# Kernel optimization log

Hardware: AMD Instinct MI355X
Metric: run time of the kernel (lower is better)

## Reference

```python
import jax, jax.numpy as jnp
import numpy as np

B, T, D = 2, 1024, 2048
E, K, H = 64, 4, 512          # n_experts, top-k, expert_dim
S, HS = 2, H * K              # shared experts, shared hidden dim
CAP = 512


def setup_inputs() -> dict:
    key = jax.random.key(0)
    ks = jax.random.split(key, 9)
    scale = 0.02
    return {
        "x": jax.random.normal(ks[0], (B, T, D), jnp.float32),
        "Wr": jax.random.normal(ks[1], (D, E), jnp.float32) * scale,
        "router_bias": jnp.zeros((E,), jnp.float32),
        "Wg": jax.random.normal(ks[2], (E, D, H), jnp.float32) * scale,
        "Wu": jax.random.normal(ks[3], (E, D, H), jnp.float32) * scale,
        "Wd": jax.random.normal(ks[4], (E, H, D), jnp.float32) * scale,
        "Sg": jax.random.normal(ks[5], (S, D, HS), jnp.float32) * scale,
        "Su": jax.random.normal(ks[6], (S, D, HS), jnp.float32) * scale,
        "Sd": jax.random.normal(ks[7], (S, HS, D), jnp.float32) * scale,
    }


def reference(x, Wr, router_bias, Wg, Wu, Wd, Sg, Su, Sd):
    Bx, Tx, Dx = x.shape
    N = Bx * Tx
    flat = x.reshape(N, Dx)                              # [N, D]

    # ---- router ----
    logits = flat @ Wr + router_bias                     # [N, E]
    scores = jax.nn.softmax(logits, axis=-1)
    topk_scores, topk_idx = jax.lax.top_k(scores, K)     # [N, K]
    topk_scores = topk_scores / topk_scores.sum(-1, keepdims=True)

    eid = topk_idx.reshape(-1)                           # [N*K] expert per assignment
    w = topk_scores.reshape(-1)                          # [N*K] combine weight
    tok = jnp.repeat(jnp.arange(N), K)                   # [N*K] source token id

    # position of each assignment within its expert's buffer
    oh = jax.nn.one_hot(eid, E, dtype=jnp.int32)         # [N*K, E]
    pos = ((jnp.cumsum(oh, axis=0) * oh).sum(-1) - 1)    # [N*K]
    valid = pos < CAP

    # ---- dispatch: scatter tokens into per-expert buffers ----
    xb = jnp.zeros((E, CAP, Dx), x.dtype).at[eid, pos].set(flat[tok], mode="drop")

    # ---- grouped SwiGLU expert FFN ----
    h = jax.nn.silu(jnp.einsum("ecd,edh->ech", xb, Wg)) * jnp.einsum("ecd,edh->ech", xb, Wu)
    yb = jnp.einsum("ech,ehd->ecd", h, Wd)               # [E, CAP, D]

    # ---- combine: gather back and weighted scatter-add to tokens ----
    y = yb[eid, jnp.minimum(pos, CAP - 1)] * (w * valid)[:, None]
    out = jnp.zeros((N, Dx), x.dtype).at[tok].add(y)

    # ---- always-on shared experts ----
    hs = jax.nn.silu(jnp.einsum("nd,sdh->nsh", flat, Sg)) * jnp.einsum("nd,sdh->nsh", flat, Su)
    out = out + jnp.einsum("nsh,shd->nd", hs, Sd)

    return out.reshape(Bx, Tx, Dx)
```

## Files before the change

### kernel.cpp

```cpp
#include <hip/hip_runtime.h>
#include <hip/hip_bf16.h>
#include <stdint.h>

#define N_TOK 2048
#define DM    2048
#define NEXP  64
#define TOPK  4
#define HEXP  512
#define CAPC  512
#define NSH   2
#define HSH   2048
#define RTB   8

typedef __attribute__((ext_vector_type(8))) short short8;
typedef __attribute__((ext_vector_type(4))) float f32x4;
typedef __attribute__((ext_vector_type(4))) float f4;
typedef __attribute__((ext_vector_type(4))) unsigned uint4v;

#define GLDS16(g, l) __builtin_amdgcn_global_load_lds(                     \
    (const __attribute__((address_space(1))) void*)(g),                    \
    (__attribute__((address_space(3))) void*)(l), 16, 0, 0)

#define VMWAIT(N) asm volatile("s_waitcnt vmcnt(" #N ")" ::: "memory")
#define BARX() do { asm volatile("" ::: "memory");                          \
                    __builtin_amdgcn_s_barrier();                           \
                    asm volatile("" ::: "memory"); } while (0)

static __device__ __forceinline__ unsigned short f2bf(float f) {
  union { float f; unsigned u; } v; v.f = f;
  unsigned r = v.u + 0x7FFFu + ((v.u >> 16) & 1u);
  return (unsigned short)(r >> 16);
}

static __device__ __forceinline__ int swz_xcd(int id, int nwg) {
  return (id & 7) * (nwg >> 3) + (id >> 3);
}

__global__ __launch_bounds__(256) void k_convert(const float* __restrict__ x,
                                                 unsigned short* __restrict__ xb) {
  int i = (blockIdx.x * 256 + threadIdx.x) * 8;
  f4 a = *(const f4*)(x + i);
  f4 b = *(const f4*)(x + i + 4);
  short8 o;
  o[0]=f2bf(a[0]); o[1]=f2bf(a[1]); o[2]=f2bf(a[2]); o[3]=f2bf(a[3]);
  o[4]=f2bf(b[0]); o[5]=f2bf(b[1]); o[6]=f2bf(b[2]); o[7]=f2bf(b[3]);
  *(short8*)(xb + i) = o;
}

#define ARGMAX_ROUND(S,I)                                            \
  { float bv = v; int bi = lane;                                     \
    _Pragma("unroll")                                                \
    for (int o = 32; o; o >>= 1) {                                   \
      float ov = __shfl_xor(bv, o); int oi = __shfl_xor(bi, o);      \
      if (ov > bv || (ov == bv && oi < bi)) { bv = ov; bi = oi; }    \
    }                                                                \
    S = bv; I = bi; if (lane == bi) v = -1.f; }

__global__ __launch_bounds__(256) void k_router(const float* __restrict__ x,
    const float* __restrict__ Wr, const float* __restrict__ bias,
    int* __restrict__ cnt, int* __restrict__ lists, float* __restrict__ wlist) {
  __shared__ float part[4][RTB][64];
  __shared__ float logits[RTB][64];
  int t = threadIdx.x;
  int e = t & 63, sl = t >> 6;
  int tok0 = blockIdx.x * RTB;
  const float* xp = x + (size_t)tok0 * DM;
  float acc[RTB];
#pragma unroll
  for (int i = 0; i < RTB; ++i) acc[i] = 0.f;
  for (int d = sl * 512; d < sl * 512 + 512; ++d) {
    float w = Wr[(size_t)d * NEXP + e];
#pragma unroll
    for (int i = 0; i < RTB; ++i) acc[i] += xp[(size_t)i * DM + d] * w;
  }
#pragma unroll
  for (int i = 0; i < RTB; ++i) part[sl][i][e] = acc[i];
  __syncthreads();
  for (int i = sl; i < RTB; i += 4)
    logits[i][e] = part[0][i][e] + part[1][i][e] + part[2][i][e] + part[3][i][e] + bias[e];
  __syncthreads();
  int lane = t & 63, wv = t >> 6;
  for (int i = wv * 2; i < wv * 2 + 2; ++i) {
    float lg = logits[i][lane];
    float m = lg;
#pragma unroll
    for (int o = 32; o; o >>= 1) m = fmaxf(m, __shfl_xor(m, o));
    float p = expf(lg - m);
    float sm = p;
#pragma unroll
    for (int o = 32; o; o >>= 1) sm += __shfl_xor(sm, o);
    float v = p / sm;
    float s0, s1, s2, s3; int i0, i1, i2, i3;
    ARGMAX_ROUND(s0, i0)
    ARGMAX_ROUND(s1, i1)
    ARGMAX_ROUND(s2, i2)
    ARGMAX_ROUND(s3, i3)
    float tot = s0 + s1 + s2 + s3;
    if (lane < TOPK) {
      float myw = (lane == 0 ? s0 : lane == 1 ? s1 : lane == 2 ? s2 : s3) / tot;
      int   mye = (lane == 0 ? i0 : lane == 1 ? i1 : lane == 2 ? i2 : i3);
      int pos = atomicAdd(&cnt[mye], 1);
      if (pos < CAPC) {
        lists[mye * CAPC + pos] = tok0 + i;
        wlist[mye * CAPC + pos] = myw;
      }
    }
  }
}

__global__ void k_offs(const int* __restrict__ cnt, int* __restrict__ offs) {
  int l = threadIdx.x;
  int c = min(cnt[l], CAPC);
  int sum = c;
#pragma unroll
  for (int o = 1; o < 64; o <<= 1) {
    int ov = __shfl_up(sum, o);
    if (l >= o) sum += ov;
  }
  offs[l + 1] = sum;
  if (l == 0) offs[0] = 0;
}


static __device__ __forceinline__ short8 frag_ldA(const unsigned short* lds, int row, int kElem) {
  int byte = row * 64 + kElem * 2;
  byte ^= ((row >> 1) & 3) << 4;
  return *(const short8*)((const char*)lds + byte);
}

static __device__ __forceinline__ short8 bfragB(const float* lB, int nl, int kb) {
  const float* p = lB + kb * 32 + (nl ^ (((kb >> 3) & 1) << 4));
  float f0 = p[0],   f1 = p[32],  f2 = p[64],  f3 = p[96];
  float f4_ = p[128], f5 = p[160], f6 = p[192], f7 = p[224];
  unsigned u0, u1, u2, u3;
  asm("v_cvt_pk_bf16_f32 %0, %1, %2" : "=v"(u0) : "v"(f0),  "v"(f1));
  asm("v_cvt_pk_bf16_f32 %0, %1, %2" : "=v"(u1) : "v"(f2),  "v"(f3));
  asm("v_cvt_pk_bf16_f32 %0, %1, %2" : "=v"(u2) : "v"(f4_), "v"(f5));
  asm("v_cvt_pk_bf16_f32 %0, %1, %2" : "=v"(u3) : "v"(f6),  "v"(f7));
  uint4v uv = {u0, u1, u2, u3};
  return __builtin_bit_cast(short8, uv);
}

static __device__ __forceinline__ void mma1f(const unsigned short* lA, const float* lB,
    f32x4 (&acc)[4][2], int wm, int lane) {
  int r16 = lane & 15;
  int kb  = (lane >> 4) * 8;
  short8 a[4], b[2];
#pragma unroll
  for (int mf = 0; mf < 4; ++mf) a[mf] = frag_ldA(lA, wm + mf * 16 + r16, kb);
#pragma unroll
  for (int nf = 0; nf < 2; ++nf) b[nf] = bfragB(lB, nf * 16 + r16, kb);
#pragma unroll
  for (int mf = 0; mf < 4; ++mf)
#pragma unroll
    for (int nf = 0; nf < 2; ++nf)
      acc[mf][nf] = __builtin_amdgcn_mfma_f32_16x16x32_bf16(a[mf], b[nf], acc[mf][nf], 0, 0, 0);
}

static __device__ __forceinline__ void mma2f(const unsigned short* lA,
    const float* lBg, const float* lBu,
    f32x4 (&accg)[4][2], f32x4 (&accu)[4][2], int wm, int lane) {
  int r16 = lane & 15;
  int kb  = (lane >> 4) * 8;
  short8 a[4], bg[2], bu[2];
#pragma unroll
  for (int mf = 0; mf < 4; ++mf) a[mf] = frag_ldA(lA, wm + mf * 16 + r16, kb);
#pragma unroll
  for (int nf = 0; nf < 2; ++nf) {
    bg[nf] = bfragB(lBg, nf * 16 + r16, kb);
    bu[nf] = bfragB(lBu, nf * 16 + r16, kb);
  }
#pragma unroll
  for (int mf = 0; mf < 4; ++mf)
#pragma unroll
    for (int nf = 0; nf < 2; ++nf) {
      accg[mf][nf] = __builtin_amdgcn_mfma_f32_16x16x32_bf16(a[mf], bg[nf], accg[mf][nf], 0, 0, 0);
      accu[mf][nf] = __builtin_amdgcn_mfma_f32_16x16x32_bf16(a[mf], bu[nf], accu[mf][nf], 0, 0, 0);
    }
}

static __device__ __forceinline__ float silu_mul(float g, float u) {
  return g / (1.f + expf(-g)) * u;
}

#define A_SETUP(asrc, SROW_EXPR)                                            \
  const unsigned short* asrc[4];                                            \
  { _Pragma("unroll")                                                       \
    for (int p = 0; p < 4; ++p) {                                           \
      int row = wv * 64 + p * 16 + (lane >> 2);                             \
      int srow = (SROW_EXPR);                                               \
      asrc[p] = Abase + (size_t)srow * lda                                  \
              + (((lane & 3) ^ ((row >> 1) & 3)) << 3);                     \
    } }
#define A_STAGE(asrc, lAbuf, k0)                                            \
  { _Pragma("unroll")                                                       \
    for (int p = 0; p < 4; ++p)                                             \
      GLDS16(asrc[p] + (k0), (lAbuf) + wv * 2048 + p * 512); }

#define B_SETUP(bsrc, Bbase, ldb)                                           \
  const float* bsrc;                                                        \
  { int k = wv * 8 + (lane >> 3);                                           \
    int c = (lane & 7) ^ (((k >> 3) & 1) << 2);                             \
    bsrc = (Bbase) + (size_t)k * (ldb) + n0 + c * 4; }
#define B_STAGE(bsrc, lBbuf, k0, ldb)                                       \
  GLDS16((bsrc) + (size_t)(k0) * (ldb), (lBbuf) + wv * 256)

__global__ __launch_bounds__(256, 3) void k_expert_gateup(const unsigned short* __restrict__ xbf,
    const float* __restrict__ Wg, const float* __restrict__ Wu,
    const int* __restrict__ cnt, const int* __restrict__ offs,
    const int* __restrict__ lists, unsigned short* __restrict__ hws) {
  int bid = swz_xcd(blockIdx.x, NEXP * (HEXP / 32));
  int e  = bid >> 4;
  int n0 = (bid & 15) * 32;
  int ne = min(cnt[e], CAPC);
  if (ne == 0) return;
  const float* Bg = Wg + (size_t)e * DM * HEXP;
  const float* Bu = Wu + (size_t)e * DM * HEXP;
  const int* lst = lists + e * CAPC;
  int base = offs[e];
  __shared__ unsigned short lA[2][256 * 32];
  __shared__ float lBg[2][32 * 32];
  __shared__ float lBu[2][32 * 32];
  int tid = threadIdx.x;
  int lane = tid & 63, wv = tid >> 6;
  int wm = wv * 64;
  const unsigned short* Abase = xbf; const int lda = DM;
  B_SETUP(bgsrc, Bg, HEXP)
  B_SETUP(busrc, Bu, HEXP)
  const int NT = DM / 32;
  for (int m0 = 0; m0 < ne; m0 += 256) {
    A_SETUP(asrc, lst[min(m0 + row, ne - 1)])
    f32x4 accg[4][2] = {};
    f32x4 accu[4][2] = {};
    A_STAGE(asrc, lA[0], 0)  B_STAGE(bgsrc, lBg[0], 0, HEXP);  B_STAGE(busrc, lBu[0], 0, HEXP);
    A_STAGE(asrc, lA[1], 32) B_STAGE(bgsrc, lBg[1], 32, HEXP); B_STAGE(busrc, lBu[1], 32, HEXP);
    VMWAIT(6); BARX();
#pragma unroll 1
    for (int t = 0; t < NT; t += 2) {
      mma2f(lA[0], lBg[0], lBu[0], accg, accu, wm, lane);
      BARX();
      if (t + 2 < NT) {
        int k2 = (t + 2) * 32;
        A_STAGE(asrc, lA[0], k2) B_STAGE(bgsrc, lBg[0], k2, HEXP); B_STAGE(busrc, lBu[0], k2, HEXP);
        VMWAIT(6);
      } else { VMWAIT(0); }
      BARX();
      mma2f(lA[1], lBg[1], lBu[1], accg, accu, wm, lane);
      if (t + 2 < NT) {
        BARX();
        if (t + 3 < NT) {
          int k3 = (t + 3) * 32;
          A_STAGE(asrc, lA[1], k3) B_STAGE(bgsrc, lBg[1], k3, HEXP); B_STAGE(busrc, lBu[1], k3, HEXP);
          VMWAIT(6);
        } else { VMWAIT(0); }
        BARX();
      }
    }
    BARX();
#pragma unroll
    for (int mf = 0; mf < 4; ++mf)
#pragma unroll
      for (int r = 0; r < 4; ++r) {
        int rl = m0 + wm + mf * 16 + (lane >> 4) * 4 + r;
        if (rl < ne) {
#pragma unroll
          for (int nf = 0; nf < 2; ++nf) {
            int col = n0 + nf * 16 + (lane & 15);
            float h = silu_mul(accg[mf][nf][r], accu[mf][nf][r]);
            hws[(size_t)(base + rl) * HEXP + col] = f2bf(h);
          }
        }
      }
  }
}

__global__ __launch_bounds__(256, 3) void k_shared_gateup(const unsigned short* __restrict__ xbf,
    const float* __restrict__ Sg, const float* __restrict__ Su,
    unsigned short* __restrict__ hs) {
  int bid = swz_xcd(blockIdx.x, NSH * (N_TOK / 256) * (HSH / 32));
  int nb = bid & 63, mb = (bid >> 6) & 7, s = bid >> 9;
  int n0 = nb * 32, m0 = mb * 256;
  const float* Bg = Sg + (size_t)s * DM * HSH;
  const float* Bu = Su + (size_t)s * DM * HSH;
  __shared__ unsigned short lA[2][256 * 32];
  __shared__ float lBg[2][32 * 32];
  __shared__ float lBu[2][32 * 32];
  int tid = threadIdx.x;
  int lane = tid & 63, wv = tid >> 6;
  int wm = wv * 64;
  const unsigned short* Abase = xbf; const int lda = DM;
  B_SETUP(bgsrc, Bg, HSH)
  B_SETUP(busrc, Bu, HSH)
  A_SETUP(asrc, m0 + row)
  f32x4 accg[4][2] = {};
  f32x4 accu[4][2] = {};
  const int NT = DM / 32;
  A_STAGE(asrc, lA[0], 0)  B_STAGE(bgsrc, lBg[0], 0, HSH);  B_STAGE(busrc, lBu[0], 0, HSH);
  A_STAGE(asrc, lA[1], 32) B_STAGE(bgsrc, lBg[1], 32, HSH); B_STAGE(busrc, lBu[1], 32, HSH);
  VMWAIT(6); BARX();
#pragma unroll 1
  for (int t = 0; t < NT; t += 2) {
    mma2f(lA[0], lBg[0], lBu[0], accg, accu, wm, lane);
    BARX();
    if (t + 2 < NT) {
      int k2 = (t + 2) * 32;
      A_STAGE(asrc, lA[0], k2) B_STAGE(bgsrc, lBg[0], k2, HSH); B_STAGE(busrc, lBu[0], k2, HSH);
      VMWAIT(6);
    } else { VMWAIT(0); }
    BARX();
    mma2f(lA[1], lBg[1], lBu[1], accg, accu, wm, lane);
    if (t + 2 < NT) {
      BARX();
      if (t + 3 < NT) {
        int k3 = (t + 3) * 32;
        A_STAGE(asrc, lA[1], k3) B_STAGE(bgsrc, lBg[1], k3, HSH); B_STAGE(busrc, lBu[1], k3, HSH);
        VMWAIT(6);
      } else { VMWAIT(0); }
      BARX();
    }
  }
#pragma unroll
  for (int mf = 0; mf < 4; ++mf)
#pragma unroll
    for (int nf = 0; nf < 2; ++nf)
#pragma unroll
      for (int r = 0; r < 4; ++r) {
        int row = m0 + wm + mf * 16 + (lane >> 4) * 4 + r;
        int col = n0 + nf * 16 + (lane & 15);
        float h = silu_mul(accg[mf][nf][r], accu[mf][nf][r]);
        hs[(size_t)row * (NSH * HSH) + s * HSH + col] = f2bf(h);
      }
}

__global__ __launch_bounds__(256, 4) void k_shared_down(const unsigned short* __restrict__ hs,
    const float* __restrict__ Sd, float* __restrict__ out) {
  int bid = swz_xcd(blockIdx.x, (N_TOK / 256) * (DM / 32));
  int nb = bid & 63, mb = bid >> 6;
  int n0 = nb * 32, m0 = mb * 256;
  __shared__ unsigned short lA[2][256 * 32];
  __shared__ float lB[2][32 * 32];
  int tid = threadIdx.x;
  int lane = tid & 63, wv = tid >> 6;
  int wm = wv * 64;
  const unsigned short* Abase = hs; const int lda = NSH * HSH;
  B_SETUP(bsrc, Sd, DM)
  A_SETUP(asrc, m0 + row)
  f32x4 acc[4][2] = {};
  const int NT = (NSH * HSH) / 32;
  A_STAGE(asrc, lA[0], 0)  B_STAGE(bsrc, lB[0], 0, DM);
  A_STAGE(asrc, lA[1], 32) B_STAGE(bsrc, lB[1], 32, DM);
  VMWAIT(5); BARX();
#pragma unroll 1
  for (int t = 0; t < NT; t += 2) {
    mma1f(lA[0], lB[0], acc, wm, lane);
    BARX();
    if (t + 2 < NT) {
      int k2 = (t + 2) * 32;
      A_STAGE(asrc, lA[0], k2) B_STAGE(bsrc, lB[0], k2, DM);
      VMWAIT(5);
    } else { VMWAIT(0); }
    BARX();
    mma1f(lA[1], lB[1], acc, wm, lane);
    if (t + 2 < NT) {
      BARX();
      if (t + 3 < NT) {
        int k3 = (t + 3) * 32;
        A_STAGE(asrc, lA[1], k3) B_STAGE(bsrc, lB[1], k3, DM);
        VMWAIT(5);
      } else { VMWAIT(0); }
      BARX();
    }
  }
#pragma unroll
  for (int mf = 0; mf < 4; ++mf)
#pragma unroll
    for (int nf = 0; nf < 2; ++nf)
#pragma unroll
      for (int r = 0; r < 4; ++r) {
        int row = m0 + wm + mf * 16 + (lane >> 4) * 4 + r;
        int col = n0 + nf * 16 + (lane & 15);
        out[(size_t)row * DM + col] = acc[mf][nf][r];
      }
}

__global__ __launch_bounds__(256, 4) void k_expert_down(const unsigned short* __restrict__ hws,
    const float* __restrict__ Wd, const int* __restrict__ cnt, const int* __restrict__ offs,
    const int* __restrict__ lists, const float* __restrict__ wlist,
    float* __restrict__ out) {
  int bid = swz_xcd(blockIdx.x, NEXP * (DM / 32));
  int e  = bid >> 6;
  int n0 = (bid & 63) * 32;
  int ne = min(cnt[e], CAPC);
  if (ne == 0) return;
  const float* B = Wd + (size_t)e * HEXP * DM;
  __shared__ unsigned short lA[2][256 * 32];
  __shared__ float lB[2][32 * 32];
  int tid = threadIdx.x;
  int lane = tid & 63, wv = tid >> 6;
  int wm = wv * 64;
  const unsigned short* Abase = hws + (size_t)offs[e] * HEXP; const int lda = HEXP;
  B_SETUP(bsrc, B, DM)
  const int NT = HEXP / 32;
  for (int m0 = 0; m0 < ne; m0 += 256) {
    A_SETUP(asrc, min(m0 + row, ne - 1))
    f32x4 acc[4][2] = {};
    A_STAGE(asrc, lA[0], 0)  B_STAGE(bsrc, lB[0], 0, DM);
    A_STAGE(asrc, lA[1], 32) B_STAGE(bsrc, lB[1], 32, DM);
    VMWAIT(5); BARX();
#pragma unroll 1
    for (int t = 0; t < NT; t += 2) {
      mma1f(lA[0], lB[0], acc, wm, lane);
      BARX();
      if (t + 2 < NT) {
        int k2 = (t + 2) * 32;
        A_STAGE(asrc, lA[0], k2) B_STAGE(bsrc, lB[0], k2, DM);
        VMWAIT(5);
      } else { VMWAIT(0); }
      BARX();
      mma1f(lA[1], lB[1], acc, wm, lane);
      if (t + 2 < NT) {
        BARX();
        if (t + 3 < NT) {
          int k3 = (t + 3) * 32;
          A_STAGE(asrc, lA[1], k3) B_STAGE(bsrc, lB[1], k3, DM);
          VMWAIT(5);
        } else { VMWAIT(0); }
        BARX();
      }
    }
    BARX();
#pragma unroll
    for (int mf = 0; mf < 4; ++mf)
#pragma unroll
      for (int r = 0; r < 4; ++r) {
        int rl = m0 + wm + mf * 16 + (lane >> 4) * 4 + r;
        if (rl < ne) {
          int tok  = lists[e * CAPC + rl];
          float w  = wlist[e * CAPC + rl];
#pragma unroll
          for (int nf = 0; nf < 2; ++nf) {
            int col = n0 + nf * 16 + (lane & 15);
            atomicAdd(out + (size_t)tok * DM + col, acc[mf][nf][r] * w);
          }
        }
      }
  }
}

extern "C" void kernel_launch(void* const* d_in, const int* in_sizes, int n_in,
                              void* d_out, int out_size, void* d_ws, size_t ws_size,
                              hipStream_t stream) {
  const float* x    = (const float*)d_in[0];
  const float* Wr   = (const float*)d_in[1];
  const float* bias = (const float*)d_in[2];
  const float* Wg   = (const float*)d_in[3];
  const float* Wu   = (const float*)d_in[4];
  const float* Wd   = (const float*)d_in[5];
  const float* Sg   = (const float*)d_in[6];
  const float* Su   = (const float*)d_in[7];
  const float* Sd   = (const float*)d_in[8];
  float* out = (float*)d_out;
  char* ws = (char*)d_ws;

  const size_t off_cnt   = 0;
  const size_t off_offs  = 256;
  const size_t off_lists = 1024;
  const size_t off_wlist = off_lists + (size_t)NEXP * CAPC * 4;
  const size_t off_xbf   = off_wlist + (size_t)NEXP * CAPC * 4;
  const size_t off_hs    = off_xbf + (size_t)N_TOK * DM * 2;
  const size_t off_h     = off_hs + (size_t)N_TOK * NSH * HSH * 2;
  const size_t req       = off_h + (size_t)N_TOK * TOPK * HEXP * 2;
  if (ws_size < req) return;

  int* cnt            = (int*)(ws + off_cnt);
  int* offs           = (int*)(ws + off_offs);
  int* lists          = (int*)(ws + off_lists);
  float* wlist        = (float*)(ws + off_wlist);
  unsigned short* xbf = (unsigned short*)(ws + off_xbf);
  unsigned short* hs  = (unsigned short*)(ws + off_hs);
  unsigned short* hws = (unsigned short*)(ws + off_h);

  hipMemsetAsync(cnt, 0, NEXP * sizeof(int), stream);
  k_convert<<<(N_TOK * DM) / (256 * 8), 256, 0, stream>>>(x, xbf);
  k_router<<<N_TOK / RTB, 256, 0, stream>>>(x, Wr, bias, cnt, lists, wlist);
  k_offs<<<1, 64, 0, stream>>>(cnt, offs);
  k_expert_gateup<<<NEXP * (HEXP / 32), 256, 0, stream>>>(xbf, Wg, Wu, cnt, offs, lists, hws);
  k_shared_gateup<<<NSH * (N_TOK / 256) * (HSH / 32), 256, 0, stream>>>(xbf, Sg, Su, hs);
  k_shared_down<<<(N_TOK / 256) * (DM / 32), 256, 0, stream>>>(hs, Sd, out);
  k_expert_down<<<NEXP * (DM / 32), 256, 0, stream>>>(hws, Wd, cnt, offs, lists, wlist, out);
}
```

Measured before the change: 731.2 us.

## Make GEMM waves independent: per-wave LDS A tiles, register-loaded B, no barriers

Restructures all four expert/shared GEMM kernels so each wave stages only its own 64-row A tile in private LDS and loads its B fragment (fp32 weights) directly from global into registers. This removes every workgroup barrier and the shared B tile in LDS. The N tile shrinks from 32 to 16 columns, which doubles the grid, and occupancy is raised to 4 blocks/CU. In exchange, B weights are fetched as strided scalar global loads with poor coalescing, and A reuse across columns drops because each block now covers fewer output columns.

```diff
diff --git a/kernel.cpp b/kernel.cpp
--- a/kernel.cpp
+++ b/kernel.cpp
@@ -22,9 +22,7 @@
     (__attribute__((address_space(3))) void*)(l), 16, 0, 0)
 
 #define VMWAIT(N) asm volatile("s_waitcnt vmcnt(" #N ")" ::: "memory")
-#define BARX() do { asm volatile("" ::: "memory");                          \
-                    __builtin_amdgcn_s_barrier();                           \
-                    asm volatile("" ::: "memory"); } while (0)
+#define LGKM0()   asm volatile("s_waitcnt lgkmcnt(0)" ::: "memory")
 
 static __device__ __forceinline__ unsigned short f2bf(float f) {
   union { float f; unsigned u; } v; v.f = f;
@@ -128,307 +126,277 @@
   return *(const short8*)((const char*)lds + byte);
 }
 
-static __device__ __forceinline__ short8 bfragB(const float* lB, int nl, int kb) {
-  const float* p = lB + kb * 32 + (nl ^ (((kb >> 3) & 1) << 4));
-  float f0 = p[0],   f1 = p[32],  f2 = p[64],  f3 = p[96];
-  float f4_ = p[128], f5 = p[160], f6 = p[192], f7 = p[224];
+static __device__ __forceinline__ short8 bfrag(const float (&b)[8]) {
   unsigned u0, u1, u2, u3;
-  asm("v_cvt_pk_bf16_f32 %0, %1, %2" : "=v"(u0) : "v"(f0),  "v"(f1));
-  asm("v_cvt_pk_bf16_f32 %0, %1, %2" : "=v"(u1) : "v"(f2),  "v"(f3));
-  asm("v_cvt_pk_bf16_f32 %0, %1, %2" : "=v"(u2) : "v"(f4_), "v"(f5));
-  asm("v_cvt_pk_bf16_f32 %0, %1, %2" : "=v"(u3) : "v"(f6),  "v"(f7));
+  asm("v_cvt_pk_bf16_f32 %0, %1, %2" : "=v"(u0) : "v"(b[0]), "v"(b[1]));
+  asm("v_cvt_pk_bf16_f32 %0, %1, %2" : "=v"(u1) : "v"(b[2]), "v"(b[3]));
+  asm("v_cvt_pk_bf16_f32 %0, %1, %2" : "=v"(u2) : "v"(b[4]), "v"(b[5]));
+  asm("v_cvt_pk_bf16_f32 %0, %1, %2" : "=v"(u3) : "v"(b[6]), "v"(b[7]));
   uint4v uv = {u0, u1, u2, u3};
   return __builtin_bit_cast(short8, uv);
 }
 
-static __device__ __forceinline__ void mma1f(const unsigned short* lA, const float* lB,
-    f32x4 (&acc)[4][2], int wm, int lane) {
-  int r16 = lane & 15;
-  int kb  = (lane >> 4) * 8;
-  short8 a[4], b[2];
-#pragma unroll
-  for (int mf = 0; mf < 4; ++mf) a[mf] = frag_ldA(lA, wm + mf * 16 + r16, kb);
-#pragma unroll
-  for (int nf = 0; nf < 2; ++nf) b[nf] = bfragB(lB, nf * 16 + r16, kb);
-#pragma unroll
-  for (int mf = 0; mf < 4; ++mf)
-#pragma unroll
-    for (int nf = 0; nf < 2; ++nf)
-      acc[mf][nf] = __builtin_amdgcn_mfma_f32_16x16x32_bf16(a[mf], b[nf], acc[mf][nf], 0, 0, 0);
-}
-
-static __device__ __forceinline__ void mma2f(const unsigned short* lA,
-    const float* lBg, const float* lBu,
-    f32x4 (&accg)[4][2], f32x4 (&accu)[4][2], int wm, int lane) {
-  int r16 = lane & 15;
-  int kb  = (lane >> 4) * 8;
-  short8 a[4], bg[2], bu[2];
-#pragma unroll
-  for (int mf = 0; mf < 4; ++mf) a[mf] = frag_ldA(lA, wm + mf * 16 + r16, kb);
-#pragma unroll
-  for (int nf = 0; nf < 2; ++nf) {
-    bg[nf] = bfragB(lBg, nf * 16 + r16, kb);
-    bu[nf] = bfragB(lBu, nf * 16 + r16, kb);
-  }
-#pragma unroll
-  for (int mf = 0; mf < 4; ++mf)
-#pragma unroll
-    for (int nf = 0; nf < 2; ++nf) {
-      accg[mf][nf] = __builtin_amdgcn_mfma_f32_16x16x32_bf16(a[mf], bg[nf], accg[mf][nf], 0, 0, 0);
-      accu[mf][nf] = __builtin_amdgcn_mfma_f32_16x16x32_bf16(a[mf], bu[nf], accu[mf][nf], 0, 0, 0);
-    }
-}
-
 static __device__ __forceinline__ float silu_mul(float g, float u) {
   return g / (1.f + expf(-g)) * u;
 }
 
 #define A_SETUP(asrc, SROW_EXPR)                                            \
   const unsigned short* asrc[4];                                            \
-  { _Pragma("unroll")                                                       \
-    for (int p = 0; p < 4; ++p) {                                           \
-      int row = wv * 64 + p * 16 + (lane >> 2);                             \
+  { _Pragma("unroll") for (int p = 0; p < 4; ++p) {                         \
+      int row = p * 16 + (lane >> 2);                                       \
       int srow = (SROW_EXPR);                                               \
       asrc[p] = Abase + (size_t)srow * lda                                  \
-              + (((lane & 3) ^ ((row >> 1) & 3)) << 3);                     \
-    } }
-#define A_STAGE(asrc, lAbuf, k0)                                            \
-  { _Pragma("unroll")                                                       \
-    for (int p = 0; p < 4; ++p)                                             \
-      GLDS16(asrc[p] + (k0), (lAbuf) + wv * 2048 + p * 512); }
-
-#define B_SETUP(bsrc, Bbase, ldb)                                           \
-  const float* bsrc;                                                        \
-  { int k = wv * 8 + (lane >> 3);                                           \
-    int c = (lane & 7) ^ (((k >> 3) & 1) << 2);                             \
-    bsrc = (Bbase) + (size_t)k * (ldb) + n0 + c * 4; }
-#define B_STAGE(bsrc, lBbuf, k0, ldb)                                       \
-  GLDS16((bsrc) + (size_t)(k0) * (ldb), (lBbuf) + wv * 256)
-
-__global__ __launch_bounds__(256, 3) void k_expert_gateup(const unsigned short* __restrict__ xbf,
+              + (((lane & 3) ^ ((row >> 1) & 3)) << 3); } }
+
+#define A_ISSUE(P, k0)                                                      \
+  { _Pragma("unroll") for (int p = 0; p < 4; ++p)                           \
+      GLDS16(asrc[p] + (k0), &lA[wv][P][0] + p * 512); }
+
+#define B_LOAD(dst, Bl, kt, ldb)                                            \
+  { _Pragma("unroll") for (int j = 0; j < 8; ++j)                           \
+      dst[j] = (Bl)[((size_t)(kt) * 32 + j) * (size_t)(ldb)]; }
+
+__global__ __launch_bounds__(256, 4) void k_expert_gateup(const unsigned short* __restrict__ xbf,
     const float* __restrict__ Wg, const float* __restrict__ Wu,
     const int* __restrict__ cnt, const int* __restrict__ offs,
     const int* __restrict__ lists, unsigned short* __restrict__ hws) {
-  int bid = swz_xcd(blockIdx.x, NEXP * (HEXP / 32));
-  int e  = bid >> 4;
-  int n0 = (bid & 15) * 32;
+  int bid = swz_xcd(blockIdx.x, NEXP * (HEXP / 16));
+  int e  = bid >> 5;
+  int n0 = (bid & 31) * 16;
   int ne = min(cnt[e], CAPC);
   if (ne == 0) return;
-  const float* Bg = Wg + (size_t)e * DM * HEXP;
-  const float* Bu = Wu + (size_t)e * DM * HEXP;
   const int* lst = lists + e * CAPC;
   int base = offs[e];
-  __shared__ unsigned short lA[2][256 * 32];
-  __shared__ float lBg[2][32 * 32];
-  __shared__ float lBu[2][32 * 32];
-  int tid = threadIdx.x;
-  int lane = tid & 63, wv = tid >> 6;
+  __shared__ unsigned short lA[4][2][2048];
+  int lane = threadIdx.x & 63, wv = threadIdx.x >> 6;
   int wm = wv * 64;
+  int r16 = lane & 15;
+  int kbm = (lane >> 4) * 8;
   const unsigned short* Abase = xbf; const int lda = DM;
-  B_SETUP(bgsrc, Bg, HEXP)
-  B_SETUP(busrc, Bu, HEXP)
+  const float* Bgl = Wg + (size_t)e * DM * HEXP + (size_t)kbm * HEXP + n0 + r16;
+  const float* Bul = Wu + (size_t)e * DM * HEXP + (size_t)kbm * HEXP + n0 + r16;
   const int NT = DM / 32;
   for (int m0 = 0; m0 < ne; m0 += 256) {
-    A_SETUP(asrc, lst[min(m0 + row, ne - 1)])
-    f32x4 accg[4][2] = {};
-    f32x4 accu[4][2] = {};
-    A_STAGE(asrc, lA[0], 0)  B_STAGE(bgsrc, lBg[0], 0, HEXP);  B_STAGE(busrc, lBu[0], 0, HEXP);
-    A_STAGE(asrc, lA[1], 32) B_STAGE(bgsrc, lBg[1], 32, HEXP); B_STAGE(busrc, lBu[1], 32, HEXP);
-    VMWAIT(6); BARX();
+    if (m0 + wm >= ne) continue;
+    A_SETUP(asrc, lst[min(m0 + wm + row, ne - 1)])
+    f32x4 accg[4] = {}; f32x4 accu[4] = {};
+    float bg0[8], bu0[8], bg1[8], bu1[8];
+    A_ISSUE(0, 0)  B_LOAD(bg0, Bgl, 0, HEXP) B_LOAD(bu0, Bul, 0, HEXP)
+    A_ISSUE(1, 32) B_LOAD(bg1, Bgl, 1, HEXP) B_LOAD(bu1, Bul, 1, HEXP)
 #pragma unroll 1
     for (int t = 0; t < NT; t += 2) {
-      mma2f(lA[0], lBg[0], lBu[0], accg, accu, wm, lane);
-      BARX();
+      VMWAIT(20);
+      {
+        short8 fg = bfrag(bg0), fu = bfrag(bu0);
+#pragma unroll
+        for (int mf = 0; mf < 4; ++mf) {
+          short8 av = frag_ldA(&lA[wv][0][0], mf * 16 + r16, kbm);
+          accg[mf] = __builtin_amdgcn_mfma_f32_16x16x32_bf16(av, fg, accg[mf], 0, 0, 0);
+          accu[mf] = __builtin_amdgcn_mfma_f32_16x16x32_bf16(av, fu, accu[mf], 0, 0, 0);
+        }
+      }
+      LGKM0();
       if (t + 2 < NT) {
-        int k2 = (t + 2) * 32;
-        A_STAGE(asrc, lA[0], k2) B_STAGE(bgsrc, lBg[0], k2, HEXP); B_STAGE(busrc, lBu[0], k2, HEXP);
-        VMWAIT(6);
+        A_ISSUE(0, (t + 2) * 32) B_LOAD(bg0, Bgl, t + 2, HEXP) B_LOAD(bu0, Bul, t + 2, HEXP)
+        VMWAIT(20);
       } else { VMWAIT(0); }
-      BARX();
-      mma2f(lA[1], lBg[1], lBu[1], accg, accu, wm, lane);
-      if (t + 2 < NT) {
-        BARX();
-        if (t + 3 < NT) {
-          int k3 = (t + 3) * 32;
-          A_STAGE(asrc, lA[1], k3) B_STAGE(bgsrc, lBg[1], k3, HEXP); B_STAGE(busrc, lBu[1], k3, HEXP);
-          VMWAIT(6);
-        } else { VMWAIT(0); }
-        BARX();
-      }
-    }
-    BARX();
+      {
+        short8 fg = bfrag(bg1), fu = bfrag(bu1);
+#pragma unroll
+        for (int mf = 0; mf < 4; ++mf) {
+          short8 av = frag_ldA(&lA[wv][1][0], mf * 16 + r16, kbm);
+          accg[mf] = __builtin_amdgcn_mfma_f32_16x16x32_bf16(av, fg, accg[mf], 0, 0, 0);
+          accu[mf] = __builtin_amdgcn_mfma_f32_16x16x32_bf16(av, fu, accu[mf], 0, 0, 0);
+        }
+      }
+      LGKM0();
+      if (t + 3 < NT) {
+        A_ISSUE(1, (t + 3) * 32) B_LOAD(bg1, Bgl, t + 3, HEXP) B_LOAD(bu1, Bul, t + 3, HEXP)
+      }
+    }
 #pragma unroll
     for (int mf = 0; mf < 4; ++mf)
 #pragma unroll
       for (int r = 0; r < 4; ++r) {
         int rl = m0 + wm + mf * 16 + (lane >> 4) * 4 + r;
         if (rl < ne) {
-#pragma unroll
-          for (int nf = 0; nf < 2; ++nf) {
-            int col = n0 + nf * 16 + (lane & 15);
-            float h = silu_mul(accg[mf][nf][r], accu[mf][nf][r]);
-            hws[(size_t)(base + rl) * HEXP + col] = f2bf(h);
-          }
-        }
-      }
-  }
-}
-
-__global__ __launch_bounds__(256, 3) void k_shared_gateup(const unsigned short* __restrict__ xbf,
+          float h = silu_mul(accg[mf][r], accu[mf][r]);
+          hws[(size_t)(base + rl) * HEXP + n0 + r16] = f2bf(h);
+        }
+      }
+  }
+}
+
+__global__ __launch_bounds__(256, 4) void k_shared_gateup(const unsigned short* __restrict__ xbf,
     const float* __restrict__ Sg, const float* __restrict__ Su,
     unsigned short* __restrict__ hs) {
-  int bid = swz_xcd(blockIdx.x, NSH * (N_TOK / 256) * (HSH / 32));
-  int nb = bid & 63, mb = (bid >> 6) & 7, s = bid >> 9;
-  int n0 = nb * 32, m0 = mb * 256;
-  const float* Bg = Sg + (size_t)s * DM * HSH;
-  const float* Bu = Su + (size_t)s * DM * HSH;
-  __shared__ unsigned short lA[2][256 * 32];
-  __shared__ float lBg[2][32 * 32];
-  __shared__ float lBu[2][32 * 32];
-  int tid = threadIdx.x;
-  int lane = tid & 63, wv = tid >> 6;
+  int bid = swz_xcd(blockIdx.x, NSH * (N_TOK / 256) * (HSH / 16));
+  int nb = bid & 127, mb = (bid >> 7) & 7, s = bid >> 10;
+  int n0 = nb * 16, m0 = mb * 256;
+  __shared__ unsigned short lA[4][2][2048];
+  int lane = threadIdx.x & 63, wv = threadIdx.x >> 6;
   int wm = wv * 64;
+  int r16 = lane & 15;
+  int kbm = (lane >> 4) * 8;
   const unsigned short* Abase = xbf; const int lda = DM;
-  B_SETUP(bgsrc, Bg, HSH)
-  B_SETUP(busrc, Bu, HSH)
-  A_SETUP(asrc, m0 + row)
-  f32x4 accg[4][2] = {};
-  f32x4 accu[4][2] = {};
+  const float* Bgl = Sg + (size_t)s * DM * HSH + (size_t)kbm * HSH + n0 + r16;
+  const float* Bul = Su + (size_t)s * DM * HSH + (size_t)kbm * HSH + n0 + r16;
   const int NT = DM / 32;
-  A_STAGE(asrc, lA[0], 0)  B_STAGE(bgsrc, lBg[0], 0, HSH);  B_STAGE(busrc, lBu[0], 0, HSH);
-  A_STAGE(asrc, lA[1], 32) B_STAGE(bgsrc, lBg[1], 32, HSH); B_STAGE(busrc, lBu[1], 32, HSH);
-  VMWAIT(6); BARX();
+  A_SETUP(asrc, m0 + wm + row)
+  f32x4 accg[4] = {}; f32x4 accu[4] = {};
+  float bg0[8], bu0[8], bg1[8], bu1[8];
+  A_ISSUE(0, 0)  B_LOAD(bg0, Bgl, 0, HSH) B_LOAD(bu0, Bul, 0, HSH)
+  A_ISSUE(1, 32) B_LOAD(bg1, Bgl, 1, HSH) B_LOAD(bu1, Bul, 1, HSH)
 #pragma unroll 1
   for (int t = 0; t < NT; t += 2) {
-    mma2f(lA[0], lBg[0], lBu[0], accg, accu, wm, lane);
-    BARX();
+    VMWAIT(20);
+    {
+      short8 fg = bfrag(bg0), fu = bfrag(bu0);
+#pragma unroll
+      for (int mf = 0; mf < 4; ++mf) {
+        short8 av = frag_ldA(&lA[wv][0][0], mf * 16 + r16, kbm);
+        accg[mf] = __builtin_amdgcn_mfma_f32_16x16x32_bf16(av, fg, accg[mf], 0, 0, 0);
+        accu[mf] = __builtin_amdgcn_mfma_f32_16x16x32_bf16(av, fu, accu[mf], 0, 0, 0);
+      }
+    }
+    LGKM0();
     if (t + 2 < NT) {
-      int k2 = (t + 2) * 32;
-      A_STAGE(asrc, lA[0], k2) B_STAGE(bgsrc, lBg[0], k2, HSH); B_STAGE(busrc, lBu[0], k2, HSH);
-      VMWAIT(6);
+      A_ISSUE(0, (t + 2) * 32) B_LOAD(bg0, Bgl, t + 2, HSH) B_LOAD(bu0, Bul, t + 2, HSH)
+      VMWAIT(20);
     } else { VMWAIT(0); }
-    BARX();
-    mma2f(lA[1], lBg[1], lBu[1], accg, accu, wm, lane);
-    if (t + 2 < NT) {
-      BARX();
-      if (t + 3 < NT) {
-        int k3 = (t + 3) * 32;
-        A_STAGE(asrc, lA[1], k3) B_STAGE(bgsrc, lBg[1], k3, HSH); B_STAGE(busrc, lBu[1], k3, HSH);
-        VMWAIT(6);
-      } else { VMWAIT(0); }
-      BARX();
+    {
+      short8 fg = bfrag(bg1), fu = bfrag(bu1);
+#pragma unroll
+      for (int mf = 0; mf < 4; ++mf) {
+        short8 av = frag_ldA(&lA[wv][1][0], mf * 16 + r16, kbm);
+        accg[mf] = __builtin_amdgcn_mfma_f32_16x16x32_bf16(av, fg, accg[mf], 0, 0, 0);
+        accu[mf] = __builtin_amdgcn_mfma_f32_16x16x32_bf16(av, fu, accu[mf], 0, 0, 0);
+      }
+    }
+    LGKM0();
+    if (t + 3 < NT) {
+      A_ISSUE(1, (t + 3) * 32) B_LOAD(bg1, Bgl, t + 3, HSH) B_LOAD(bu1, Bul, t + 3, HSH)
     }
   }
 #pragma unroll
   for (int mf = 0; mf < 4; ++mf)
 #pragma unroll
-    for (int nf = 0; nf < 2; ++nf)
-#pragma unroll
-      for (int r = 0; r < 4; ++r) {
-        int row = m0 + wm + mf * 16 + (lane >> 4) * 4 + r;
-        int col = n0 + nf * 16 + (lane & 15);
-        float h = silu_mul(accg[mf][nf][r], accu[mf][nf][r]);
-        hs[(size_t)row * (NSH * HSH) + s * HSH + col] = f2bf(h);
-      }
+    for (int r = 0; r < 4; ++r) {
+      int row = m0 + wm + mf * 16 + (lane >> 4) * 4 + r;
+      float h = silu_mul(accg[mf][r], accu[mf][r]);
+      hs[(size_t)row * (NSH * HSH) + s * HSH + n0 + r16] = f2bf(h);
+    }
 }
 
 __global__ __launch_bounds__(256, 4) void k_shared_down(const unsigned short* __restrict__ hs,
     const float* __restrict__ Sd, float* __restrict__ out) {
-  int bid = swz_xcd(blockIdx.x, (N_TOK / 256) * (DM / 32));
-  int nb = bid & 63, mb = bid >> 6;
-  int n0 = nb * 32, m0 = mb * 256;
-  __shared__ unsigned short lA[2][256 * 32];
-  __shared__ float lB[2][32 * 32];
-  int tid = threadIdx.x;
-  int lane = tid & 63, wv = tid >> 6;
+  int bid = swz_xcd(blockIdx.x, (N_TOK / 256) * (DM / 16));
+  int nb = bid & 127, mb = bid >> 7;
+  int n0 = nb * 16, m0 = mb * 256;
+  __shared__ unsigned short lA[4][2][2048];
+  int lane = threadIdx.x & 63, wv = threadIdx.x >> 6;
   int wm = wv * 64;
+  int r16 = lane & 15;
+  int kbm = (lane >> 4) * 8;
   const unsigned short* Abase = hs; const int lda = NSH * HSH;
-  B_SETUP(bsrc, Sd, DM)
-  A_SETUP(asrc, m0 + row)
-  f32x4 acc[4][2] = {};
+  const float* Bl = Sd + (size_t)kbm * DM + n0 + r16;
   const int NT = (NSH * HSH) / 32;
-  A_STAGE(asrc, lA[0], 0)  B_STAGE(bsrc, lB[0], 0, DM);
-  A_STAGE(asrc, lA[1], 32) B_STAGE(bsrc, lB[1], 32, DM);
-  VMWAIT(5); BARX();
+  A_SETUP(asrc, m0 + wm + row)
+  f32x4 acc[4] = {};
+  float b0[8], b1[8];
+  A_ISSUE(0, 0)  B_LOAD(b0, Bl, 0, DM)
+  A_ISSUE(1, 32) B_LOAD(b1, Bl, 1, DM)
 #pragma unroll 1
   for (int t = 0; t < NT; t += 2) {
-    mma1f(lA[0], lB[0], acc, wm, lane);
-    BARX();
+    VMWAIT(12);
+    {
+      short8 fb = bfrag(b0);
+#pragma unroll
+      for (int mf = 0; mf < 4; ++mf) {
+        short8 av = frag_ldA(&lA[wv][0][0], mf * 16 + r16, kbm);
+        acc[mf] = __builtin_amdgcn_mfma_f32_16x16x32_bf16(av, fb, acc[mf], 0, 0, 0);
+      }
+    }
+    LGKM0();
     if (t + 2 < NT) {
-      int k2 = (t + 2) * 32;
-      A_STAGE(asrc, lA[0], k2) B_STAGE(bsrc, lB[0], k2, DM);
-      VMWAIT(5);
+      A_ISSUE(0, (t + 2) * 32) B_LOAD(b0, Bl, t + 2, DM)
+      VMWAIT(12);
     } else { VMWAIT(0); }
-    BARX();
-    mma1f(lA[1], lB[1], acc, wm, lane);
-    if (t + 2 < NT) {
-      BARX();
-      if (t + 3 < NT) {
-        int k3 = (t + 3) * 32;
-        A_STAGE(asrc, lA[1], k3) B_STAGE(bsrc, lB[1], k3, DM);
-        VMWAIT(5);
-      } else { VMWAIT(0); }
-      BARX();
+    {
+      short8 fb = bfrag(b1);
+#pragma unroll
+      for (int mf = 0; mf < 4; ++mf) {
+        short8 av = frag_ldA(&lA[wv][1][0], mf * 16 + r16, kbm);
+        acc[mf] = __builtin_amdgcn_mfma_f32_16x16x32_bf16(av, fb, acc[mf], 0, 0, 0);
+      }
+    }
+    LGKM0();
+    if (t + 3 < NT) {
+      A_ISSUE(1, (t + 3) * 32) B_LOAD(b1, Bl, t + 3, DM)
     }
   }
 #pragma unroll
   for (int mf = 0; mf < 4; ++mf)
 #pragma unroll
-    for (int nf = 0; nf < 2; ++nf)
-#pragma unroll
-      for (int r = 0; r < 4; ++r) {
-        int row = m0 + wm + mf * 16 + (lane >> 4) * 4 + r;
-        int col = n0 + nf * 16 + (lane & 15);
-        out[(size_t)row * DM + col] = acc[mf][nf][r];
-      }
+    for (int r = 0; r < 4; ++r) {
+      int row = m0 + wm + mf * 16 + (lane >> 4) * 4 + r;
+      out[(size_t)row * DM + n0 + r16] = acc[mf][r];
+    }
 }
 
 __global__ __launch_bounds__(256, 4) void k_expert_down(const unsigned short* __restrict__ hws,
     const float* __restrict__ Wd, const int* __restrict__ cnt, const int* __restrict__ offs,
     const int* __restrict__ lists, const float* __restrict__ wlist,
     float* __restrict__ out) {
-  int bid = swz_xcd(blockIdx.x, NEXP * (DM / 32));
-  int e  = bid >> 6;
-  int n0 = (bid & 63) * 32;
+  int bid = swz_xcd(blockIdx.x, NEXP * (DM / 16));
+  int e  = bid >> 7;
+  int n0 = (bid & 127) * 16;
   int ne = min(cnt[e], CAPC);
   if (ne == 0) return;
-  const float* B = Wd + (size_t)e * HEXP * DM;
-  __shared__ unsigned short lA[2][256 * 32];
-  __shared__ float lB[2][32 * 32];
-  int tid = threadIdx.x;
-  int lane = tid & 63, wv = tid >> 6;
+  __shared__ unsigned short lA[4][2][2048];
+  int lane = threadIdx.x & 63, wv = threadIdx.x >> 6;
   int wm = wv * 64;
+  int r16 = lane & 15;
+  int kbm = (lane >> 4) * 8;
   const unsigned short* Abase = hws + (size_t)offs[e] * HEXP; const int lda = HEXP;
-  B_SETUP(bsrc, B, DM)
+  const float* Bl = Wd + (size_t)e * HEXP * DM + (size_t)kbm * DM + n0 + r16;
   const int NT = HEXP / 32;
   for (int m0 = 0; m0 < ne; m0 += 256) {
-    A_SETUP(asrc, min(m0 + row, ne - 1))
-    f32x4 acc[4][2] = {};
-    A_STAGE(asrc, lA[0], 0)  B_STAGE(bsrc, lB[0], 0, DM);
-    A_STAGE(asrc, lA[1], 32) B_STAGE(bsrc, lB[1], 32, DM);
-    VMWAIT(5); BARX();
+    if (m0 + wm >= ne) continue;
+    A_SETUP(asrc, min(m0 + wm + row, ne - 1))
+    f32x4 acc[4] = {};
+    float b0[8], b1[8];
+    A_ISSUE(0, 0)  B_LOAD(b0, Bl, 0, DM)
+    A_ISSUE(1, 32) B_LOAD(b1, Bl, 1, DM)
 #pragma unroll 1
     for (int t = 0; t < NT; t += 2) {
-      mma1f(lA[0], lB[0], acc, wm, lane);
-      BARX();
+      VMWAIT(12);
+      {
+        short8 fb = bfrag(b0);
+#pragma unroll
+        for (int mf = 0; mf < 4; ++mf) {
+          short8 av = frag_ldA(&lA[wv][0][0], mf * 16 + r16, kbm);
+          acc[mf] = __builtin_amdgcn_mfma_f32_16x16x32_bf16(av, fb, acc[mf], 0, 0, 0);
+        }
+      }
+      LGKM0();
       if (t + 2 < NT) {
-        int k2 = (t + 2) * 32;
-        A_STAGE(asrc, lA[0], k2) B_STAGE(bsrc, lB[0], k2, DM);
-        VMWAIT(5);
+        A_ISSUE(0, (t + 2) * 32) B_LOAD(b0, Bl, t + 2, DM)
+        VMWAIT(12);
       } else { VMWAIT(0); }
-      BARX();
-      mma1f(lA[1], lB[1], acc, wm, lane);
-      if (t + 2 < NT) {
-        BARX();
-        if (t + 3 < NT) {
-          int k3 = (t + 3) * 32;
-          A_STAGE(asrc, lA[1], k3) B_STAGE(bsrc, lB[1], k3, DM);
-          VMWAIT(5);
-        } else { VMWAIT(0); }
-        BARX();
-      }
-    }
-    BARX();
+      {
+        short8 fb = bfrag(b1);
+#pragma unroll
+        for (int mf = 0; mf < 4; ++mf) {
+          short8 av = frag_ldA(&lA[wv][1][0], mf * 16 + r16, kbm);
+          acc[mf] = __builtin_amdgcn_mfma_f32_16x16x32_bf16(av, fb, acc[mf], 0, 0, 0);
+        }
+      }
+      LGKM0();
+      if (t + 3 < NT) {
+        A_ISSUE(1, (t + 3) * 32) B_LOAD(b1, Bl, t + 3, DM)
+      }
+    }
 #pragma unroll
     for (int mf = 0; mf < 4; ++mf)
 #pragma unroll
@@ -437,11 +405,7 @@
         if (rl < ne) {
           int tok  = lists[e * CAPC + rl];
           float w  = wlist[e * CAPC + rl];
-#pragma unroll
-          for (int nf = 0; nf < 2; ++nf) {
-            int col = n0 + nf * 16 + (lane & 15);
-            atomicAdd(out + (size_t)tok * DM + col, acc[mf][nf][r] * w);
-          }
+          atomicAdd(out + (size_t)tok * DM + n0 + r16, acc[mf][r] * w);
         }
       }
   }
@@ -484,8 +448,8 @@
   k_convert<<<(N_TOK * DM) / (256 * 8), 256, 0, stream>>>(x, xbf);
   k_router<<<N_TOK / RTB, 256, 0, stream>>>(x, Wr, bias, cnt, lists, wlist);
   k_offs<<<1, 64, 0, stream>>>(cnt, offs);
-  k_expert_gateup<<<NEXP * (HEXP / 32), 256, 0, stream>>>(xbf, Wg, Wu, cnt, offs, lists, hws);
-  k_shared_gateup<<<NSH * (N_TOK / 256) * (HSH / 32), 256, 0, stream>>>(xbf, Sg, Su, hs);
-  k_shared_down<<<(N_TOK / 256) * (DM / 32), 256, 0, stream>>>(hs, Sd, out);
-  k_expert_down<<<NEXP * (DM / 32), 256, 0, stream>>>(hws, Wd, cnt, offs, lists, wlist, out);
-}
+  k_expert_gateup<<<NEXP * (HEXP / 16), 256, 0, stream>>>(xbf, Wg, Wu, cnt, offs, lists, hws);
+  k_shared_gateup<<<NSH * (N_TOK / 256) * (HSH / 16), 256, 0, stream>>>(xbf, Sg, Su, hs);
+  k_shared_down<<<(N_TOK / 256) * (DM / 16), 256, 0, stream>>>(hs, Sd, out);
+  k_expert_down<<<NEXP * (DM / 16), 256, 0, stream>>>(hws, Wd, cnt, offs, lists, wlist, out);
+}
```

Measured after the change: 1.170 ms. 60.0% more time.
